# Kernel optimization log

Hardware: AMD Instinct MI355X
Metric: run time of the kernel (lower is better)

The kernel has to match this reference:

```python
import jax, jax.numpy as jnp
import numpy as np

D_IN = 1024
D_OUT = 1024
NUM_HEADS = 16
HEAD_DIM = D_OUT // NUM_HEADS


def setup_inputs() -> dict:
    key = jax.random.key(0)
    k1, k2, k3, k4 = jax.random.split(key, 4)
    x = jax.random.normal(k1, (2, 2048, D_IN), dtype=jnp.float32)
    # Linear weights stored torch-style [out_features, in_features]
    W_qkv = jax.random.normal(k2, (3 * D_OUT, D_IN), dtype=jnp.float32) * (1.0 / np.sqrt(D_IN))
    W_out = jax.random.normal(k3, (D_OUT, D_OUT), dtype=jnp.float32) * (1.0 / np.sqrt(D_OUT))
    b_out = jax.random.normal(k4, (D_OUT,), dtype=jnp.float32) * 0.01
    return {"x": x, "W_qkv": W_qkv, "W_out": W_out, "b_out": b_out}


def reference(x, W_qkv, W_out, b_out):
    b, s, _ = x.shape
    qkv = jnp.einsum('bsi,oi->bso', x, W_qkv)  # [b, s, 3*d_out]
    q, k, v = jnp.split(qkv, 3, axis=-1)
    def to_heads(t):
        return t.reshape(b, s, NUM_HEADS, HEAD_DIM).transpose(0, 2, 1, 3)
    q, k, v = to_heads(q), to_heads(k), to_heads(v)
    # NOTE: original module does NOT scale by 1/sqrt(head_dim)
    scores = jnp.einsum('bhqd,bhkd->bhqk', q, k)
    causal = jnp.tril(jnp.ones((s, s), dtype=bool))  # True = keep
    scores = jnp.where(causal[None, None], scores, -jnp.inf)
    attn = jax.nn.softmax(scores, axis=-1)
    ctx = jnp.einsum('bhqk,bhkd->bhqd', attn, v)
    ctx = ctx.transpose(0, 2, 1, 3).reshape(b, s, D_OUT)
    return jnp.einsum('bso,po->bsp', ctx, W_out) + b_out
```

## Files before the change

### kernel.cpp

```cpp
#include <hip/hip_runtime.h>
#include <cstdint>
#include <cstddef>


typedef __attribute__((ext_vector_type(8))) short bf16x8;
typedef __attribute__((ext_vector_type(4))) float f32x4;

#define LOG2E 1.44269504f

#define MFMA16(a, b, c) __builtin_amdgcn_mfma_f32_16x16x32_bf16((a), (b), (c), 0, 0, 0)

#define GLDS16(g, s)                                                        \
  __builtin_amdgcn_global_load_lds(                                         \
      (const __attribute__((address_space(1))) void*)(g),                   \
      (__attribute__((address_space(3))) void*)(s), 16, 0, 0)

#define ASYNC_BAR(N) asm volatile("s_waitcnt vmcnt(" #N ")\n\ts_barrier" ::: "memory")
#define BAR() asm volatile("s_barrier" ::: "memory")

static __device__ __forceinline__ float exp2_hw(float x) {
  float r;
  asm("v_exp_f32 %0, %1" : "=v"(r) : "v"(x));
  return r;
}
#define EXP2F(x) exp2_hw(x)

static __device__ __forceinline__ unsigned short f2bf(float f) {
  unsigned int u = __builtin_bit_cast(unsigned int, f);
  u += 0x7FFFu + ((u >> 16) & 1u);
  return (unsigned short)(u >> 16);
}

static __device__ __forceinline__ unsigned int pk2bf(float a, float b) {
  const unsigned int ua = __builtin_bit_cast(unsigned int, a) + 0x8000u;
  const unsigned int ub = __builtin_bit_cast(unsigned int, b) + 0x8000u;
  return __builtin_amdgcn_perm(ub, ua, 0x07060302);
}

__global__ __launch_bounds__(256) void cast_bf16(const float* __restrict__ x,
                                                 const float* __restrict__ wq,
                                                 const float* __restrict__ wo,
                                                 unsigned short* __restrict__ xb,
                                                 unsigned short* __restrict__ wqb,
                                                 unsigned short* __restrict__ wob)
{
  const int id = blockIdx.x * 256 + threadIdx.x;
  const float* src;
  unsigned short* dst;
  int off;
  if (id < 1048576)               { src = x;  dst = xb;  off = id; }
  else if (id < 1048576 + 786432) { src = wq; dst = wqb; off = id - 1048576; }
  else                            { src = wo; dst = wob; off = id - (1048576 + 786432); }
  float4 v = ((const float4*)src)[off];
  ushort4 o;
  o.x = f2bf(v.x); o.y = f2bf(v.y); o.z = f2bf(v.z); o.w = f2bf(v.w);
  ((ushort4*)dst)[off] = o;
}

#define MMAC(AF, BF, MS, NS)                                                       \
  do {                                                                             \
    __builtin_amdgcn_s_setprio(1);                                                 \
    if (swapped) {                                                                 \
      _Pragma("unroll")                                                            \
      for (int mt = 0; mt < 4; ++mt)                                               \
        _Pragma("unroll")                                                          \
        for (int nt = 0; nt < 2; ++nt) {                                           \
          acc[(MS)*4+mt][(NS)*2+nt] = MFMA16(BF[nt][0], AF[mt][0], acc[(MS)*4+mt][(NS)*2+nt]); \
          acc[(MS)*4+mt][(NS)*2+nt] = MFMA16(BF[nt][1], AF[mt][1], acc[(MS)*4+mt][(NS)*2+nt]); \
        }                                                                          \
    } else {                                                                       \
      _Pragma("unroll")                                                            \
      for (int mt = 0; mt < 4; ++mt)                                               \
        _Pragma("unroll")                                                          \
        for (int nt = 0; nt < 2; ++nt) {                                           \
          acc[(MS)*4+mt][(NS)*2+nt] = MFMA16(AF[mt][0], BF[nt][0], acc[(MS)*4+mt][(NS)*2+nt]); \
          acc[(MS)*4+mt][(NS)*2+nt] = MFMA16(AF[mt][1], BF[nt][1], acc[(MS)*4+mt][(NS)*2+nt]); \
        }                                                                          \
    }                                                                              \
    __builtin_amdgcn_s_setprio(0);                                                 \
  } while (0)

__global__ __launch_bounds__(512, 2) void gemm_qkv(const unsigned short* __restrict__ A,
                                                   const unsigned short* __restrict__ B,
                                                   unsigned short* __restrict__ Qb,
                                                   unsigned short* __restrict__ Kb,
                                                   unsigned short* __restrict__ Vt)
{
  __shared__ unsigned short pool[65536];

  const int tid  = threadIdx.x;
  const int wave = tid >> 6, lane = tid & 63, quad = lane >> 4, cl = lane & 15;
  const int wm = wave >> 2, wn = wave & 3;

  const int bid = blockIdx.x;
  const int xcd = bid & 7, j = bid >> 3;
  const int mb = (xcd >> 1) * 4 + j / 6;
  const int nb = (xcd & 1) * 6 + j % 6;
  const int m0 = mb * 256, n0 = nb * 256;
  const int part = nb >> 2;
  const bool swapped = (part < 2);

  const int lrow = lane >> 3;
  const int sg   = (lane & 7) ^ lrow;

  auto stageA = [&](int h0, int buf, int k0) {
    #pragma unroll
    for (int ii = 0; ii < 2; ++ii) {
      const int r0 = h0 + wave * 16 + ii * 8;
      GLDS16(A + (size_t)(m0 + r0 + lrow) * 1024 + k0 + sg * 8,
             &pool[buf * 32768 + r0 * 64]);
    }
  };
  auto stageB = [&](int h0, int buf, int k0) {
    #pragma unroll
    for (int ii = 0; ii < 2; ++ii) {
      const int r0 = h0 + wave * 16 + ii * 8;
      GLDS16(B + (size_t)(n0 + r0 + lrow) * 1024 + k0 + sg * 8,
             &pool[buf * 32768 + 16384 + r0 * 64]);
    }
  };

  const int rswz = cl & 7;
  auto loadA = [&](bf16x8 (&af)[4][2], int msub, int b) {
    const unsigned short* base = &pool[b * 32768];
    #pragma unroll
    for (int mt = 0; mt < 4; ++mt) {
      const int row = wm * 128 + msub * 64 + mt * 16 + cl;
      #pragma unroll
      for (int kk = 0; kk < 2; ++kk)
        af[mt][kk] = *(const bf16x8*)&base[row * 64 + ((kk * 4 + quad) ^ rswz) * 8];
    }
  };
  auto loadB = [&](bf16x8 (&bf)[2][2], int nsub, int b) {
    const unsigned short* base = &pool[b * 32768 + 16384];
    #pragma unroll
    for (int nt = 0; nt < 2; ++nt) {
      const int row = wn * 64 + nsub * 32 + nt * 16 + cl;
      #pragma unroll
      for (int kk = 0; kk < 2; ++kk)
        bf[nt][kk] = *(const bf16x8*)&base[row * 64 + ((kk * 4 + quad) ^ rswz) * 8];
    }
  };

  f32x4 acc[8][4];
  #pragma unroll
  for (int i = 0; i < 8; ++i)
    #pragma unroll
    for (int jj = 0; jj < 4; ++jj)
      #pragma unroll
      for (int r = 0; r < 4; ++r) acc[i][jj][r] = 0.f;

  stageB(0,   0, 0);
  stageA(0,   0, 0);
  stageB(128, 0, 0);
  stageA(128, 0, 0);
  stageB(0,   1, 64);
  stageA(0,   1, 64);

  #pragma unroll 1
  for (int t = 0; t < 16; ++t) {
    const int b = t & 1, bn = b ^ 1;
    const int kc  = (t + 1) * 64;
    const int kc2 = (t + 2) * 64;

    bf16x8 af[4][2], bfA[2][2], bfB[2][2];

    if (t < 15) { ASYNC_BAR(4); } else { ASYNC_BAR(0); }
    loadA(af, 0, b);
    loadB(bfA, 0, b);
    if (t < 15) stageB(128, bn, kc);
    MMAC(af, bfA, 0, 0);

    loadB(bfB, 1, b);
    if (t < 15) stageA(128, bn, kc);
    MMAC(af, bfB, 0, 1);

    BAR();
    loadA(af, 1, b);
    if (t < 14) stageB(0, b, kc2);
    MMAC(af, bfB, 1, 1);

    BAR();
    if (t < 14) stageA(0, b, kc2);
    MMAC(af, bfA, 1, 0);
  }

  const int bb = m0 >> 11, ss = m0 & 2047;
  if (part < 2) {
    unsigned short* dst = (part == 0) ? Qb : Kb;
    const float sc2 = (part == 0) ? LOG2E : 1.0f;
    const int npb = (n0 & 1023) + wn * 64;
    #pragma unroll
    for (int mt = 0; mt < 8; ++mt) {
      const int m = ss + wm * 128 + mt * 16 + cl;
      #pragma unroll
      for (int nt = 0; nt < 4; ++nt) {
        const int np = npb + nt * 16 + quad * 4;
        const int hh = np >> 6, d0 = np & 63;
        ushort4 pk;
        pk.x = f2bf(acc[mt][nt][0] * sc2);
        pk.y = f2bf(acc[mt][nt][1] * sc2);
        pk.z = f2bf(acc[mt][nt][2] * sc2);
        pk.w = f2bf(acc[mt][nt][3] * sc2);
        *(ushort4*)&dst[((size_t)(bb * 16 + hh) * 2048 + m) * 64 + d0] = pk;
      }
    }
  } else {
    unsigned short* trans = pool;
    #pragma unroll 1
    for (int r = 0; r < 2; ++r) {
      __syncthreads();
      if ((wn >> 1) == r) {
        #pragma unroll
        for (int mt = 0; mt < 8; ++mt) {
          const int s_l = wm * 128 + mt * 16 + quad * 4;
          #pragma unroll
          for (int nt = 0; nt < 4; ++nt) {
            const int n_l = (wn & 1) * 64 + nt * 16 + cl;
            ushort4 pk;
            pk.x = f2bf(acc[mt][nt][0]); pk.y = f2bf(acc[mt][nt][1]);
            pk.z = f2bf(acc[mt][nt][2]); pk.w = f2bf(acc[mt][nt][3]);
            *(ushort4*)&trans[n_l * 264 + s_l] = pk;
          }
        }
      }
      __syncthreads();
      const int row = tid >> 2, q4 = tid & 3;
      const int nv = (n0 & 1023) + r * 128 + row;
      const int hh = nv >> 6, d = nv & 63;
      unsigned short* drow = Vt + ((size_t)(bb * 16 + hh) * 64 + d) * 2048 + ss + q4 * 64;
      #pragma unroll
      for (int i = 0; i < 8; ++i)
        *(bf16x8*)(drow + i * 8) = *(const bf16x8*)&trans[row * 264 + q4 * 64 + i * 8];
    }
  }
}

__global__ __launch_bounds__(256) void gemm_out(const unsigned short* __restrict__ A,
                                                const unsigned short* __restrict__ B,
                                                const float* __restrict__ bias,
                                                float* __restrict__ OutF)
{
  __shared__ unsigned short pool[18432];

  const int tid  = threadIdx.x;
  const int wave = tid >> 6, lane = tid & 63, quad = lane >> 4, cl = lane & 15;
  const int m0 = blockIdx.y * 128, n0 = blockIdx.x * 64;
  const int sr = lane >> 2, sc = lane & 3;

  f32x4 acc[2][4];
  #pragma unroll
  for (int i = 0; i < 2; ++i)
    #pragma unroll
    for (int j = 0; j < 4; ++j)
      #pragma unroll
      for (int r = 0; r < 4; ++r) acc[i][j][r] = 0.f;

  const int scs = (sc ^ ((sr >> 1) & 3)) * 8;
  const int rchunk = (quad ^ ((cl >> 1) & 3)) * 8;

  auto stage = [&](int k0, int buf) {
    unsigned short* As = pool + buf * 6144;
    unsigned short* Bs = As + 4096;
    #pragma unroll
    for (int ii = 0; ii < 2; ++ii) {
      const int r = wave * 32 + ii * 16 + sr;
      GLDS16(A + (size_t)(m0 + r) * 1024 + k0 + scs, &As[(wave * 32 + ii * 16) * 32]);
    }
    const int rB = wave * 16 + sr;
    GLDS16(B + (size_t)(n0 + rB) * 1024 + k0 + scs, &Bs[(wave * 16) * 32]);
  };

  stage(0, 0);
  stage(32, 1);
  int cur = 0;
  #pragma unroll 1
  for (int it = 0; it < 32; ++it) {
    if (it + 2 < 32) {
      ASYNC_BAR(3);
      const int bnx = (cur == 0) ? 2 : cur - 1;
      stage((it + 2) * 32, bnx);
    } else if (it + 1 < 32) {
      ASYNC_BAR(3);
    } else {
      ASYNC_BAR(0);
    }

    const unsigned short* As = pool + cur * 6144;
    const unsigned short* Bs = As + 4096;
    bf16x8 af[2], bfr[4];
    #pragma unroll
    for (int mt = 0; mt < 2; ++mt)
      af[mt] = *(const bf16x8*)&As[(wave * 32 + mt * 16 + cl) * 32 + rchunk];
    #pragma unroll
    for (int nt = 0; nt < 4; ++nt)
      bfr[nt] = *(const bf16x8*)&Bs[(nt * 16 + cl) * 32 + rchunk];

    __builtin_amdgcn_s_setprio(1);
    #pragma unroll
    for (int mt = 0; mt < 2; ++mt)
      #pragma unroll
      for (int nt = 0; nt < 4; ++nt)
        acc[mt][nt] = MFMA16(bfr[nt], af[mt], acc[mt][nt]);
    __builtin_amdgcn_s_setprio(0);
    cur = (cur == 2) ? 0 : cur + 1;
  }

  #pragma unroll
  for (int mt = 0; mt < 2; ++mt) {
    const int m = m0 + wave * 32 + mt * 16 + cl;
    #pragma unroll
    for (int nt = 0; nt < 4; ++nt) {
      const int n = n0 + nt * 16 + quad * 4;
      const float4 bv = *(const float4*)(bias + n);
      float4 o;
      o.x = acc[mt][nt][0] + bv.x; o.y = acc[mt][nt][1] + bv.y;
      o.z = acc[mt][nt][2] + bv.z; o.w = acc[mt][nt][3] + bv.w;
      *(float4*)&OutF[(size_t)m * 1024 + n] = o;
    }
  }
}

__global__ __launch_bounds__(256) void attn_mfma(const unsigned short* __restrict__ Qb,
                                                 const unsigned short* __restrict__ Kb,
                                                 const unsigned short* __restrict__ Vt,
                                                 unsigned short* __restrict__ CTX)
{
  __shared__ unsigned short Ksm[3][64 * 64];
  __shared__ unsigned short Vsm[3][64 * 64];
  __shared__ unsigned short Psm[4][16 * 40];

  const int tid  = threadIdx.x;
  const int wave = tid >> 6, lane = tid & 63, quad = lane >> 4, cl = lane & 15;

  const int L  = blockIdx.x;
  const int bh = 4 * (L & 7) + ((L >> 3) & 3);
  const int b  = bh >> 4, h = bh & 15;
  const int pp = 31 - (L >> 5);
  const int G  = pp * 4 + wave;
  const int qb = G * 16;
  const size_t base = (size_t)bh * (2048 * 64);

  bf16x8 qf[2];
  #pragma unroll
  for (int dk = 0; dk < 2; ++dk)
    qf[dk] = *(const bf16x8*)(Qb + base + (size_t)(qb + cl) * 64 + dk * 32 + quad * 8);

  f32x4 oacc[4];
  #pragma unroll
  for (int dt = 0; dt < 4; ++dt)
    #pragma unroll
    for (int r = 0; r < 4; ++r) oacc[dt][r] = 0.f;
  float lr[4] = {};

  bf16x8 ones;
  #pragma unroll
  for (int k = 0; k < 8; ++k) ones[k] = (short)0x3F80;

  const int lrow  = lane >> 3;
  const int lslot = (lane & 7) ^ lrow;
  const int nch = pp + 1;

  auto stageKV = [&](int j64, int buf) {
    #pragma unroll
    for (int ii = 0; ii < 2; ++ii) {
      const int r0 = wave * 16 + ii * 8;
      GLDS16(Kb + base + (size_t)(j64 + r0 + lrow) * 64 + lslot * 8, &Ksm[buf][r0 * 64]);
      GLDS16(Vt + base + (size_t)(r0 + lrow) * 2048 + j64 + lslot * 8, &Vsm[buf][r0 * 64]);
    }
  };

  stageKV(0, 0);
  stageKV(64, 1);
  int cur = 0;
  #pragma unroll 1
  for (int ch = 0; ch < nch; ++ch) {
    if (ch + 2 < nch) {
      ASYNC_BAR(4);
      const int bnx = (cur == 0) ? 2 : cur - 1;
      stageKV((ch + 2) * 64, bnx);
    } else if (ch + 1 < nch) {
      ASYNC_BAR(4);
    } else {
      ASYNC_BAR(0);
    }

    const unsigned short* Kc = Ksm[cur];
    const unsigned short* Vc = Vsm[cur];

    const int j64 = ch * 64;
    #pragma unroll
    for (int jli = 0; jli < 2; ++jli) {
      const int jg0 = j64 + jli * 32;
      if (jg0 > qb + 15) continue;
      const int jl = jli * 32;

      bf16x8 kf[2][2];
      #pragma unroll
      for (int jf = 0; jf < 2; ++jf)
        #pragma unroll
        for (int dk = 0; dk < 2; ++dk) {
          const int jrow = jl + jf * 16 + cl;
          const int slot = (dk * 4 + quad) ^ (cl & 7);
          kf[jf][dk] = *(const bf16x8*)&Kc[jrow * 64 + slot * 8];
        }

      f32x4 st[2];
      __builtin_amdgcn_s_setprio(1);
      #pragma unroll
      for (int jf = 0; jf < 2; ++jf) {
        f32x4 z;
        #pragma unroll
        for (int r = 0; r < 4; ++r) z[r] = 0.f;
        z = MFMA16(kf[jf][0], qf[0], z);
        st[jf] = MFMA16(kf[jf][1], qf[1], z);
      }
      __builtin_amdgcn_s_setprio(0);

      const bool diag = (jg0 + 32 > qb);
      #pragma unroll
      for (int jf = 0; jf < 2; ++jf) {
        float pv[4];
        if (diag) {
          const int qg = qb + cl;
          #pragma unroll
          for (int r = 0; r < 4; ++r) {
            const int jg = jg0 + jf * 16 + quad * 4 + r;
            pv[r] = (jg <= qg) ? EXP2F(st[jf][r]) : 0.f;
          }
        } else {
          #pragma unroll
          for (int r = 0; r < 4; ++r) pv[r] = EXP2F(st[jf][r]);
        }
        uint2 w;
        w.x = pk2bf(pv[0], pv[1]);
        w.y = pk2bf(pv[2], pv[3]);
        *(uint2*)&Psm[wave][cl * 40 + jf * 16 + quad * 4] = w;
      }

      bf16x8 vf[4];
      #pragma unroll
      for (int dt = 0; dt < 4; ++dt) {
        const int d = dt * 16 + cl;
        const int slot = ((jl >> 3) + quad) ^ (cl & 7);
        vf[dt] = *(const bf16x8*)&Vc[d * 64 + slot * 8];
      }

      __builtin_amdgcn_s_setprio(1);
      {
        const bf16x8 pf = *(const bf16x8*)&Psm[wave][cl * 40 + quad * 8];
        f32x4 z;
        #pragma unroll
        for (int r = 0; r < 4; ++r) z[r] = 0.f;
        const f32x4 ls = MFMA16(pf, ones, z);
        #pragma unroll
        for (int r = 0; r < 4; ++r) lr[r] += ls[r];
        #pragma unroll
        for (int dt = 0; dt < 4; ++dt)
          oacc[dt] = MFMA16(pf, vf[dt], oacc[dt]);
      }
      __builtin_amdgcn_s_setprio(0);
    }
    cur = (cur == 2) ? 0 : cur + 1;
  }

  {
    float inv[4];
    #pragma unroll
    for (int r = 0; r < 4; ++r) inv[r] = 1.f / lr[r];
    #pragma unroll
    for (int dt = 0; dt < 4; ++dt)
      #pragma unroll
      for (int r = 0; r < 4; ++r)
        CTX[(size_t)(b * 2048 + qb + quad * 4 + r) * 1024 +
            h * 64 + dt * 16 + cl] = f2bf(oacc[dt][r] * inv[r]);
  }
}

extern "C" void kernel_launch(void* const* d_in, const int* in_sizes, int n_in,
                              void* d_out, int out_size, void* d_ws, size_t ws_size,
                              hipStream_t stream)
{
  const float* x    = (const float*)d_in[0];
  const float* Wqkv = (const float*)d_in[1];
  const float* Wout = (const float*)d_in[2];
  const float* bout = (const float*)d_in[3];
  float* out = (float*)d_out;

  char* ws = (char*)d_ws;
  unsigned short* xb  = (unsigned short*)(ws);
  unsigned short* wqb = (unsigned short*)(ws + 8388608);
  unsigned short* wob = (unsigned short*)(ws + 14680064);
  unsigned short* Qb  = (unsigned short*)(ws + 16777216);
  unsigned short* Kb  = (unsigned short*)(ws + 25165824);
  unsigned short* Vt  = (unsigned short*)(ws + 33554432);
  unsigned short* CTX = (unsigned short*)(ws + 41943040);

  cast_bf16<<<dim3(8192), dim3(256), 0, stream>>>(x, Wqkv, Wout, xb, wqb, wob);

  gemm_qkv<<<dim3(192), dim3(512), 0, stream>>>(xb, wqb, Qb, Kb, Vt);

  attn_mfma<<<dim3(1024), dim3(256), 0, stream>>>(Qb, Kb, Vt, CTX);

  gemm_out<<<dim3(16, 32), dim3(256), 0, stream>>>(CTX, wob, bout, out);
}
```

Before: 190.4 us.

## Double-buffer attention K/V in chunk pairs and widen output GEMM tile

The attention kernel's three-slot ring with one barrier per 64-key chunk becomes two buffers of two chunks each. It waits for all loads once per 128 keys and then prefetches the next pair, which halves the number of barriers. The trade-off is that each wait drains every outstanding load (vmcnt 0), so a round's prefetch has only that round's compute to hide behind. The output projection GEMM tile grows from 128x64 to 128x128 with a 2x2 wave layout, giving more MFMA reuse per LDS fragment load and half as many blocks (256), with higher register and LDS use per block.

```diff
diff --git a/kernel.cpp b/kernel.cpp
--- a/kernel.cpp
+++ b/kernel.cpp
@@ -236,21 +236,22 @@
   }
 }
 
-__global__ __launch_bounds__(256) void gemm_out(const unsigned short* __restrict__ A,
+__global__ __launch_bounds__(256) void gemm_obt(const unsigned short* __restrict__ A,
                                                 const unsigned short* __restrict__ B,
                                                 const float* __restrict__ bias,
                                                 float* __restrict__ OutF)
 {
-  __shared__ unsigned short pool[18432];
+  __shared__ unsigned short pool[24576];
 
   const int tid  = threadIdx.x;
   const int wave = tid >> 6, lane = tid & 63, quad = lane >> 4, cl = lane & 15;
-  const int m0 = blockIdx.y * 128, n0 = blockIdx.x * 64;
+  const int wm = wave >> 1, wn = wave & 1;
+  const int m0 = blockIdx.y * 128, n0 = blockIdx.x * 128;
   const int sr = lane >> 2, sc = lane & 3;
 
-  f32x4 acc[2][4];
+  f32x4 acc[4][4];
   #pragma unroll
-  for (int i = 0; i < 2; ++i)
+  for (int i = 0; i < 4; ++i)
     #pragma unroll
     for (int j = 0; j < 4; ++j)
       #pragma unroll
@@ -260,15 +261,14 @@
   const int rchunk = (quad ^ ((cl >> 1) & 3)) * 8;
 
   auto stage = [&](int k0, int buf) {
-    unsigned short* As = pool + buf * 6144;
+    unsigned short* As = pool + buf * 8192;
     unsigned short* Bs = As + 4096;
     #pragma unroll
     for (int ii = 0; ii < 2; ++ii) {
       const int r = wave * 32 + ii * 16 + sr;
       GLDS16(A + (size_t)(m0 + r) * 1024 + k0 + scs, &As[(wave * 32 + ii * 16) * 32]);
-    }
-    const int rB = wave * 16 + sr;
-    GLDS16(B + (size_t)(n0 + rB) * 1024 + k0 + scs, &Bs[(wave * 16) * 32]);
+      GLDS16(B + (size_t)(n0 + r) * 1024 + k0 + scs, &Bs[(wave * 32 + ii * 16) * 32]);
+    }
   };
 
   stage(0, 0);
@@ -277,28 +277,28 @@
   #pragma unroll 1
   for (int it = 0; it < 32; ++it) {
     if (it + 2 < 32) {
-      ASYNC_BAR(3);
+      ASYNC_BAR(4);
       const int bnx = (cur == 0) ? 2 : cur - 1;
       stage((it + 2) * 32, bnx);
     } else if (it + 1 < 32) {
-      ASYNC_BAR(3);
+      ASYNC_BAR(4);
     } else {
       ASYNC_BAR(0);
     }
 
-    const unsigned short* As = pool + cur * 6144;
+    const unsigned short* As = pool + cur * 8192;
     const unsigned short* Bs = As + 4096;
-    bf16x8 af[2], bfr[4];
-    #pragma unroll
-    for (int mt = 0; mt < 2; ++mt)
-      af[mt] = *(const bf16x8*)&As[(wave * 32 + mt * 16 + cl) * 32 + rchunk];
+    bf16x8 af[4], bfr[4];
+    #pragma unroll
+    for (int mt = 0; mt < 4; ++mt)
+      af[mt] = *(const bf16x8*)&As[(wm * 64 + mt * 16 + cl) * 32 + rchunk];
     #pragma unroll
     for (int nt = 0; nt < 4; ++nt)
-      bfr[nt] = *(const bf16x8*)&Bs[(nt * 16 + cl) * 32 + rchunk];
+      bfr[nt] = *(const bf16x8*)&Bs[(wn * 64 + nt * 16 + cl) * 32 + rchunk];
 
     __builtin_amdgcn_s_setprio(1);
     #pragma unroll
-    for (int mt = 0; mt < 2; ++mt)
+    for (int mt = 0; mt < 4; ++mt)
       #pragma unroll
       for (int nt = 0; nt < 4; ++nt)
         acc[mt][nt] = MFMA16(bfr[nt], af[mt], acc[mt][nt]);
@@ -307,11 +307,11 @@
   }
 
   #pragma unroll
-  for (int mt = 0; mt < 2; ++mt) {
-    const int m = m0 + wave * 32 + mt * 16 + cl;
+  for (int mt = 0; mt < 4; ++mt) {
+    const int m = m0 + wm * 64 + mt * 16 + cl;
     #pragma unroll
     for (int nt = 0; nt < 4; ++nt) {
-      const int n = n0 + nt * 16 + quad * 4;
+      const int n = n0 + wn * 64 + nt * 16 + quad * 4;
       const float4 bv = *(const float4*)(bias + n);
       float4 o;
       o.x = acc[mt][nt][0] + bv.x; o.y = acc[mt][nt][1] + bv.y;
@@ -326,8 +326,8 @@
                                                  const unsigned short* __restrict__ Vt,
                                                  unsigned short* __restrict__ CTX)
 {
-  __shared__ unsigned short Ksm[3][64 * 64];
-  __shared__ unsigned short Vsm[3][64 * 64];
+  __shared__ unsigned short Ksm[2][2][64 * 64];
+  __shared__ unsigned short Vsm[2][2][64 * 64];
   __shared__ unsigned short Psm[4][16 * 40];
 
   const int tid  = threadIdx.x;
@@ -360,108 +360,111 @@
   const int lrow  = lane >> 3;
   const int lslot = (lane & 7) ^ lrow;
   const int nch = pp + 1;
-
-  auto stageKV = [&](int j64, int buf) {
+  const int nrd = (nch + 1) >> 1;
+
+  auto stageKV = [&](int ch, int buf, int sub) {
+    const int j64 = ch * 64;
     #pragma unroll
     for (int ii = 0; ii < 2; ++ii) {
       const int r0 = wave * 16 + ii * 8;
-      GLDS16(Kb + base + (size_t)(j64 + r0 + lrow) * 64 + lslot * 8, &Ksm[buf][r0 * 64]);
-      GLDS16(Vt + base + (size_t)(r0 + lrow) * 2048 + j64 + lslot * 8, &Vsm[buf][r0 * 64]);
+      GLDS16(Kb + base + (size_t)(j64 + r0 + lrow) * 64 + lslot * 8,
+             &Ksm[buf][sub][r0 * 64]);
+      GLDS16(Vt + base + (size_t)(r0 + lrow) * 2048 + j64 + lslot * 8,
+             &Vsm[buf][sub][r0 * 64]);
     }
   };
 
-  stageKV(0, 0);
-  stageKV(64, 1);
-  int cur = 0;
+  stageKV(0, 0, 0);
+  stageKV(1, 0, 1);
+
   #pragma unroll 1
-  for (int ch = 0; ch < nch; ++ch) {
-    if (ch + 2 < nch) {
-      ASYNC_BAR(4);
-      const int bnx = (cur == 0) ? 2 : cur - 1;
-      stageKV((ch + 2) * 64, bnx);
-    } else if (ch + 1 < nch) {
-      ASYNC_BAR(4);
-    } else {
-      ASYNC_BAR(0);
-    }
-
-    const unsigned short* Kc = Ksm[cur];
-    const unsigned short* Vc = Vsm[cur];
-
-    const int j64 = ch * 64;
-    #pragma unroll
-    for (int jli = 0; jli < 2; ++jli) {
-      const int jg0 = j64 + jli * 32;
-      if (jg0 > qb + 15) continue;
-      const int jl = jli * 32;
-
-      bf16x8 kf[2][2];
-      #pragma unroll
-      for (int jf = 0; jf < 2; ++jf)
+  for (int t = 0; t < nrd; ++t) {
+    ASYNC_BAR(0);
+    if (t + 1 < nrd) {
+      stageKV(2 * t + 2, (t + 1) & 1, 0);
+      stageKV(2 * t + 3, (t + 1) & 1, 1);
+    }
+
+    #pragma unroll
+    for (int cs = 0; cs < 2; ++cs) {
+      const int ch = 2 * t + cs;
+      const unsigned short* Kc = Ksm[t & 1][cs];
+      const unsigned short* Vc = Vsm[t & 1][cs];
+      const int j64c = ch * 64;
+
+      #pragma unroll
+      for (int jli = 0; jli < 2; ++jli) {
+        const int jg0 = j64c + jli * 32;
+        if (jg0 > qb + 15) continue;
+        const int jl = jli * 32;
+
+        bf16x8 kf[2][2];
         #pragma unroll
-        for (int dk = 0; dk < 2; ++dk) {
-          const int jrow = jl + jf * 16 + cl;
-          const int slot = (dk * 4 + quad) ^ (cl & 7);
-          kf[jf][dk] = *(const bf16x8*)&Kc[jrow * 64 + slot * 8];
+        for (int jf = 0; jf < 2; ++jf)
+          #pragma unroll
+          for (int dk = 0; dk < 2; ++dk) {
+            const int jrow = jl + jf * 16 + cl;
+            const int slot = (dk * 4 + quad) ^ (cl & 7);
+            kf[jf][dk] = *(const bf16x8*)&Kc[jrow * 64 + slot * 8];
+          }
+
+        f32x4 st[2];
+        __builtin_amdgcn_s_setprio(1);
+        #pragma unroll
+        for (int jf = 0; jf < 2; ++jf) {
+          f32x4 z;
+          #pragma unroll
+          for (int r = 0; r < 4; ++r) z[r] = 0.f;
+          z = MFMA16(kf[jf][0], qf[0], z);
+          st[jf] = MFMA16(kf[jf][1], qf[1], z);
         }
-
-      f32x4 st[2];
-      __builtin_amdgcn_s_setprio(1);
-      #pragma unroll
-      for (int jf = 0; jf < 2; ++jf) {
-        f32x4 z;
+        __builtin_amdgcn_s_setprio(0);
+
+        const bool diag = (jg0 + 32 > qb);
         #pragma unroll
-        for (int r = 0; r < 4; ++r) z[r] = 0.f;
-        z = MFMA16(kf[jf][0], qf[0], z);
-        st[jf] = MFMA16(kf[jf][1], qf[1], z);
+        for (int jf = 0; jf < 2; ++jf) {
+          float pv[4];
+          if (diag) {
+            const int qg = qb + cl;
+            #pragma unroll
+            for (int r = 0; r < 4; ++r) {
+              const int jg = jg0 + jf * 16 + quad * 4 + r;
+              pv[r] = (jg <= qg) ? EXP2F(st[jf][r]) : 0.f;
+            }
+          } else {
+            #pragma unroll
+            for (int r = 0; r < 4; ++r) pv[r] = EXP2F(st[jf][r]);
+          }
+          uint2 w;
+          w.x = pk2bf(pv[0], pv[1]);
+          w.y = pk2bf(pv[2], pv[3]);
+          *(uint2*)&Psm[wave][cl * 40 + jf * 16 + quad * 4] = w;
+        }
+
+        bf16x8 vf[4];
+        #pragma unroll
+        for (int dt = 0; dt < 4; ++dt) {
+          const int d = dt * 16 + cl;
+          const int slot = ((jl >> 3) + quad) ^ (cl & 7);
+          vf[dt] = *(const bf16x8*)&Vc[d * 64 + slot * 8];
+        }
+
+        __builtin_amdgcn_s_setprio(1);
+        {
+          const bf16x8 pf = *(const bf16x8*)&Psm[wave][cl * 40 + quad * 8];
+          f32x4 z;
+          #pragma unroll
+          for (int r = 0; r < 4; ++r) z[r] = 0.f;
+          const f32x4 ls = MFMA16(pf, ones, z);
+          #pragma unroll
+          for (int r = 0; r < 4; ++r) lr[r] += ls[r];
+          #pragma unroll
+          for (int dt = 0; dt < 4; ++dt)
+            oacc[dt] = MFMA16(pf, vf[dt], oacc[dt]);
+        }
+        __builtin_amdgcn_s_setprio(0);
       }
-      __builtin_amdgcn_s_setprio(0);
-
-      const bool diag = (jg0 + 32 > qb);
-      #pragma unroll
-      for (int jf = 0; jf < 2; ++jf) {
-        float pv[4];
-        if (diag) {
-          const int qg = qb + cl;
-          #pragma unroll
-          for (int r = 0; r < 4; ++r) {
-            const int jg = jg0 + jf * 16 + quad * 4 + r;
-            pv[r] = (jg <= qg) ? EXP2F(st[jf][r]) : 0.f;
-          }
-        } else {
-          #pragma unroll
-          for (int r = 0; r < 4; ++r) pv[r] = EXP2F(st[jf][r]);
-        }
-        uint2 w;
-        w.x = pk2bf(pv[0], pv[1]);
-        w.y = pk2bf(pv[2], pv[3]);
-        *(uint2*)&Psm[wave][cl * 40 + jf * 16 + quad * 4] = w;
-      }
-
-      bf16x8 vf[4];
-      #pragma unroll
-      for (int dt = 0; dt < 4; ++dt) {
-        const int d = dt * 16 + cl;
-        const int slot = ((jl >> 3) + quad) ^ (cl & 7);
-        vf[dt] = *(const bf16x8*)&Vc[d * 64 + slot * 8];
-      }
-
-      __builtin_amdgcn_s_setprio(1);
-      {
-        const bf16x8 pf = *(const bf16x8*)&Psm[wave][cl * 40 + quad * 8];
-        f32x4 z;
-        #pragma unroll
-        for (int r = 0; r < 4; ++r) z[r] = 0.f;
-        const f32x4 ls = MFMA16(pf, ones, z);
-        #pragma unroll
-        for (int r = 0; r < 4; ++r) lr[r] += ls[r];
-        #pragma unroll
-        for (int dt = 0; dt < 4; ++dt)
-          oacc[dt] = MFMA16(pf, vf[dt], oacc[dt]);
-      }
-      __builtin_amdgcn_s_setprio(0);
-    }
-    cur = (cur == 2) ? 0 : cur + 1;
+    }
   }
 
   {
@@ -502,5 +505,5 @@
 
   attn_mfma<<<dim3(1024), dim3(256), 0, stream>>>(Qb, Kb, Vt, CTX);
 
-  gemm_out<<<dim3(16, 32), dim3(256), 0, stream>>>(CTX, wob, bout, out);
-}
+  gemm_obt<<<dim3(8, 32), dim3(256), 0, stream>>>(CTX, wob, bout, out);
+}
```

Result: faster. 185.3 us (-2.7%).
